# Kernel optimization log

Hardware: AMD Instinct MI355X
Metric: run time of the kernel (lower is better)

Reference implementation:

```python
import jax, jax.numpy as jnp
import numpy as np

N_USER, N_FOOD, N_ING, N_CAT, N_HAB = 50000, 30000, 20000, 5000, 10000
N_NODES = N_USER + N_FOOD + N_ING + N_CAT + N_HAB  # 115000
N_REL = 8
COMMON = 128
HIDDEN = 128
N_CLASSES = 2
N_EDGES = 1500000


def setup_inputs() -> dict:
    key = jax.random.key(0)
    ks = jax.random.split(key, 24)

    def lin(k, din, dout):
        k1, k2 = jax.random.split(k)
        s = 1.0 / np.sqrt(din)
        W = jax.random.uniform(k1, (din, dout), jnp.float32, -s, s)
        b = jax.random.uniform(k2, (dout,), jnp.float32, -s, s)
        return W, b

    Wu, bu = lin(ks[0], 256, COMMON)
    Wf, bf = lin(ks[1], 512, COMMON)
    Wi, bi = lin(ks[2], 128, COMMON)
    Wc, bc = lin(ks[3], 64, COMMON)
    Wh, bh = lin(ks[4], 64, COMMON)

    s1 = 1.0 / np.sqrt(COMMON)
    W1 = jax.random.uniform(ks[5], (N_REL, COMMON, HIDDEN), jnp.float32, -s1, s1)
    root1 = jax.random.uniform(ks[6], (COMMON, HIDDEN), jnp.float32, -s1, s1)
    b1 = jnp.zeros((HIDDEN,), jnp.float32)

    s2 = 1.0 / np.sqrt(HIDDEN)
    W2 = jax.random.uniform(ks[7], (N_REL, HIDDEN, N_CLASSES), jnp.float32, -s2, s2)
    root2 = jax.random.uniform(ks[8], (HIDDEN, N_CLASSES), jnp.float32, -s2, s2)
    b2 = jnp.zeros((N_CLASSES,), jnp.float32)

    return {
        "x_user": jax.random.normal(ks[9], (N_USER, 256), jnp.float32),
        "x_food": jax.random.normal(ks[10], (N_FOOD, 512), jnp.float32),
        "x_ingredient": jax.random.normal(ks[11], (N_ING, 128), jnp.float32),
        "x_category": jax.random.normal(ks[12], (N_CAT, 64), jnp.float32),
        "x_habit": jax.random.normal(ks[13], (N_HAB, 64), jnp.float32),
        "Wu": Wu, "bu": bu, "Wf": Wf, "bf": bf, "Wi": Wi, "bi": bi,
        "Wc": Wc, "bc": bc, "Wh": Wh, "bh": bh,
        "W1": W1, "root1": root1, "b1": b1,
        "W2": W2, "root2": root2, "b2": b2,
        "edge_index": jax.random.randint(ks[14], (2, N_EDGES), 0, N_NODES, jnp.int64),
        "edge_type": jax.random.randint(ks[15], (N_EDGES,), 0, N_REL, jnp.int64),
    }


def rgcn_conv(x, src, dst, etype, W, root, bias):
    # x: [N, Din]; W: [R, Din, Dout]. Per-relation node transform, then
    # per-edge gather + per-(dst, relation) mean aggregation (PyG RGCNConv, aggr='mean').
    N = x.shape[0]
    R = W.shape[0]
    h = jnp.einsum('nd,rdf->nrf', x, W)            # [N, R, Dout]
    msgs = h[src, etype]                           # [E, Dout]
    seg = dst * R + etype                          # combined (dst, relation) segment id
    sums = jax.ops.segment_sum(msgs, seg, num_segments=N * R)
    cnt = jax.ops.segment_sum(jnp.ones((src.shape[0],), x.dtype), seg, num_segments=N * R)
    mean = sums / jnp.maximum(cnt, 1.0)[:, None]   # [N*R, Dout]
    agg = mean.reshape(N, R, -1).sum(axis=1)       # sum over relations
    return agg + x @ root + bias


def reference(x_user, x_food, x_ingredient, x_category, x_habit,
              Wu, bu, Wf, bf, Wi, bi, Wc, bc, Wh, bh,
              W1, root1, b1, W2, root2, b2,
              edge_index, edge_type):
    x_all = jnp.concatenate([
        x_user @ Wu + bu,
        x_food @ Wf + bf,
        x_ingredient @ Wi + bi,
        x_category @ Wc + bc,
        x_habit @ Wh + bh,
    ], axis=0)                                     # [N, COMMON]
    src, dst = edge_index[0], edge_index[1]
    x = rgcn_conv(x_all, src, dst, edge_type, W1, root1, b1)
    x = jax.nn.relu(x)                             # dropout is identity in eval mode
    x = rgcn_conv(x, src, dst, edge_type, W2, root2, b2)
    return jax.nn.log_softmax(x, axis=1)
```

## Files before the change

### kernel.cpp

```cpp
#include <hip/hip_runtime.h>
#include <hip/hip_bf16.h>
#include <math.h>

#define NU 50000
#define NFOOD 30000
#define NING 20000
#define NCAT 5000
#define NHAB 10000
#define NNODES 115000
#define NCHUNK 14375
#define NREL 8
#define NSEG (NNODES * NREL)
#define NEDGE 1500000
#define SCAN_B 256

typedef __attribute__((ext_vector_type(8))) short short8;
typedef __attribute__((ext_vector_type(4))) float f32x4;

static inline size_t alignup(size_t x) { return (x + 255) & ~(size_t)255; }

__device__ inline float bf16_bits_to_f32(unsigned short u) {
  return __uint_as_float(((unsigned)u) << 16);
}
__device__ inline unsigned short f32_to_bf16_bits(float f) {
  unsigned u = __float_as_uint(f);
  unsigned r = u + 0x7fffu + ((u >> 16) & 1u);
  return (unsigned short)(r >> 16);
}
__device__ inline unsigned pack_bf16x2(float lo, float hi) {
  return (unsigned)f32_to_bf16_bits(lo) | ((unsigned)f32_to_bf16_bits(hi) << 16);
}

template <bool A_F32, bool OUT_BF16, bool RELU_OUT>
__global__ __launch_bounds__(256) void mfma_gemm(
    const void* __restrict__ Ain, const unsigned short* __restrict__ Bt, int ldB,
    const float* __restrict__ bias, void* __restrict__ Cv, int ldC, int Nstore,
    int M, int N, int K) {
  __shared__ char As[128 * 128];
  __shared__ char Bs[128 * 128];
  const int tid = threadIdx.x;
  const int lane = tid & 63;
  const int wv = tid >> 6;
  const int bm = blockIdx.y * 128;
  const int bn = blockIdx.x * 128;
  f32x4 acc[2][8] = {};

  for (int k0 = 0; k0 < K; k0 += 64) {
    if (A_F32) {
      const float* A = (const float*)Ain;
#pragma unroll
      for (int it = 0; it < 4; ++it) {
        int u = it * 256 + tid;
        int m = u >> 3, c = u & 7;
        int mg = bm + m; if (mg >= M) mg = M - 1;
        const float4* src = (const float4*)(A + (size_t)mg * K + k0 + c * 8);
        float4 lo4 = src[0], hi4 = src[1];
        unsigned q0 = pack_bf16x2(lo4.x, lo4.y);
        unsigned q1 = pack_bf16x2(lo4.z, lo4.w);
        unsigned q2 = pack_bf16x2(hi4.x, hi4.y);
        unsigned q3 = pack_bf16x2(hi4.z, hi4.w);
        int off = m * 128 + ((c * 16) ^ ((m & 7) << 4));
        *(int4*)(As + off) = make_int4(q0, q1, q2, q3);
      }
    } else {
      const unsigned short* A = (const unsigned short*)Ain;
#pragma unroll
      for (int it = 0; it < 4; ++it) {
        int u = it * 256 + tid;
        int m = u >> 3, c = u & 7;
        int mg = bm + m; if (mg >= M) mg = M - 1;
        int4 v = *(const int4*)((const char*)(A + (size_t)mg * K + k0) + c * 16);
        int off = m * 128 + ((c * 16) ^ ((m & 7) << 4));
        *(int4*)(As + off) = v;
      }
    }
#pragma unroll
    for (int it = 0; it < 4; ++it) {
      int u = it * 256 + tid;
      int n = u >> 3, c = u & 7;
      int4 v = *(const int4*)((const char*)(Bt + (size_t)(bn + n) * ldB + k0) + c * 16);
      int off = n * 128 + ((c * 16) ^ ((n & 7) << 4));
      *(int4*)(Bs + off) = v;
    }
    __syncthreads();
#pragma unroll
    for (int kk = 0; kk < 2; ++kk) {
      int kbyte = kk * 64 + ((lane >> 4) << 4);
      short8 af[2];
#pragma unroll
      for (int mi = 0; mi < 2; ++mi) {
        int m = wv * 32 + mi * 16 + (lane & 15);
        af[mi] = *(const short8*)(As + m * 128 + (kbyte ^ ((m & 7) << 4)));
      }
#pragma unroll
      for (int ni = 0; ni < 8; ++ni) {
        int n = ni * 16 + (lane & 15);
        short8 bf = *(const short8*)(Bs + n * 128 + (kbyte ^ ((n & 7) << 4)));
#pragma unroll
        for (int mi = 0; mi < 2; ++mi)
          acc[mi][ni] = __builtin_amdgcn_mfma_f32_16x16x32_bf16(af[mi], bf, acc[mi][ni], 0, 0, 0);
      }
    }
    __syncthreads();
  }
#pragma unroll
  for (int mi = 0; mi < 2; ++mi) {
#pragma unroll
    for (int r = 0; r < 4; ++r) {
      int row = bm + wv * 32 + mi * 16 + ((lane >> 4) << 2) + r;
      if (row < M) {
#pragma unroll
        for (int ni = 0; ni < 8; ++ni) {
          int col = bn + ni * 16 + (lane & 15);
          if (col < Nstore) {
            float v = acc[mi][ni][r] + (bias ? bias[col] : 0.f);
            if (RELU_OUT) v = fmaxf(v, 0.f);
            if (OUT_BF16)
              ((unsigned short*)Cv)[(size_t)row * ldC + col] = f32_to_bf16_bits(v);
            else
              ((float*)Cv)[(size_t)row * ldC + col] = v;
          }
        }
      }
    }
  }
}

__global__ __launch_bounds__(256) void l1_gemm(
    const unsigned short* __restrict__ M9, const unsigned short* __restrict__ xall,
    const unsigned short* __restrict__ W1rT, const float* __restrict__ b1,
    unsigned short* __restrict__ x1, int d0, int Mc) {
  __shared__ char As[128 * 128];
  __shared__ char Bs[128 * 128];
  const int tid = threadIdx.x;
  const int lane = tid & 63;
  const int wv = tid >> 6;
  const int bm = blockIdx.y * 128;
  f32x4 acc[2][8] = {};

  for (int k0 = 0; k0 < 1152; k0 += 64) {
#pragma unroll
    for (int it = 0; it < 4; ++it) {
      int u = it * 256 + tid;
      int m = u >> 3, c = u & 7;
      int mg = bm + m; if (mg >= Mc) mg = Mc - 1;
      const char* src;
      if (k0 < 1024) src = (const char*)(M9 + (size_t)mg * 1024 + k0) + c * 16;
      else src = (const char*)(xall + (size_t)(d0 + mg) * 128 + (k0 - 1024)) + c * 16;
      int4 v = *(const int4*)src;
      int off = m * 128 + ((c * 16) ^ ((m & 7) << 4));
      *(int4*)(As + off) = v;
    }
#pragma unroll
    for (int it = 0; it < 4; ++it) {
      int u = it * 256 + tid;
      int n = u >> 3, c = u & 7;
      int4 v = *(const int4*)((const char*)(W1rT + (size_t)n * 1152 + k0) + c * 16);
      int off = n * 128 + ((c * 16) ^ ((n & 7) << 4));
      *(int4*)(Bs + off) = v;
    }
    __syncthreads();
#pragma unroll
    for (int kk = 0; kk < 2; ++kk) {
      int kbyte = kk * 64 + ((lane >> 4) << 4);
      short8 af[2];
#pragma unroll
      for (int mi = 0; mi < 2; ++mi) {
        int m = wv * 32 + mi * 16 + (lane & 15);
        af[mi] = *(const short8*)(As + m * 128 + (kbyte ^ ((m & 7) << 4)));
      }
#pragma unroll
      for (int ni = 0; ni < 8; ++ni) {
        int n = ni * 16 + (lane & 15);
        short8 bf = *(const short8*)(Bs + n * 128 + (kbyte ^ ((n & 7) << 4)));
#pragma unroll
        for (int mi = 0; mi < 2; ++mi)
          acc[mi][ni] = __builtin_amdgcn_mfma_f32_16x16x32_bf16(af[mi], bf, acc[mi][ni], 0, 0, 0);
      }
    }
    __syncthreads();
  }
#pragma unroll
  for (int mi = 0; mi < 2; ++mi) {
#pragma unroll
    for (int r = 0; r < 4; ++r) {
      int row = bm + wv * 32 + mi * 16 + ((lane >> 4) << 2) + r;
      if (row < Mc) {
#pragma unroll
        for (int ni = 0; ni < 8; ++ni) {
          int col = ni * 16 + (lane & 15);
          float v = fmaxf(acc[mi][ni][r] + b1[col], 0.f);
          x1[(size_t)(d0 + row) * 128 + col] = f32_to_bf16_bits(v);
        }
      }
    }
  }
}

__global__ void build_Bt(const float* __restrict__ W, unsigned short* __restrict__ Wt,
                         int K, int N) {
  int idx = blockIdx.x * blockDim.x + threadIdx.x;
  if (idx >= N * K) return;
  int n = idx / K, k = idx - n * K;
  Wt[idx] = f32_to_bf16_bits(W[(size_t)k * N + n]);
}

__global__ void build_W1rT(const float* __restrict__ W1, const float* __restrict__ root1,
                           unsigned short* __restrict__ Wt) {
  int idx = blockIdx.x * blockDim.x + threadIdx.x;
  if (idx >= 128 * 1152) return;
  int f = idx / 1152, c = idx - f * 1152;
  float v;
  if (c < 1024) { int t = c >> 7, k = c & 127; v = W1[((size_t)t * 128 + k) * 128 + f]; }
  else { int k = c - 1024; v = root1[(size_t)k * 128 + f]; }
  Wt[idx] = f32_to_bf16_bits(v);
}

__global__ void build_B2pad(const float* __restrict__ W2, const float* __restrict__ root2,
                            unsigned short* __restrict__ Bt) {
  int idx = blockIdx.x * blockDim.x + threadIdx.x;
  if (idx >= 128 * 128) return;
  int n = idx >> 7, k = idx & 127;
  float v = 0.f;
  if (n < 16) v = W2[((size_t)(n >> 1) * 128 + k) * 2 + (n & 1)];
  else if (n < 18) v = root2[(size_t)k * 2 + (n - 16)];
  Bt[idx] = f32_to_bf16_bits(v);
}

__global__ void count_dt_xcd(const int* __restrict__ ei, const int* __restrict__ et,
                             int* __restrict__ cnt_dt) {
  int cls = blockIdx.x & 7;
  unsigned lo = cls * NCHUNK, hi = lo + NCHUNK;
  int e = (blockIdx.x >> 3) * blockDim.x + threadIdx.x;
  int stride = (gridDim.x >> 3) * blockDim.x;
  for (; e < NEDGE; e += stride) {
    unsigned d = (unsigned)ei[NEDGE + e]; if (d >= NNODES) d = 0;
    if (d < lo || d >= hi) continue;
    unsigned t = (unsigned)et[e]; if (t >= NREL) t = 0;
    atomicAdd(cnt_dt + d * NREL + t, 1);
  }
}

__global__ void scan_block(const int* __restrict__ in, int* __restrict__ out,
                           int* __restrict__ bsum, int n) {
  __shared__ int s[SCAN_B];
  int i = blockIdx.x * SCAN_B + threadIdx.x;
  int x = (i < n) ? in[i] : 0;
  s[threadIdx.x] = x;
  __syncthreads();
  for (int d = 1; d < SCAN_B; d <<= 1) {
    int v = (threadIdx.x >= d) ? s[threadIdx.x - d] : 0;
    __syncthreads();
    s[threadIdx.x] += v;
    __syncthreads();
  }
  if (i < n) out[i] = s[threadIdx.x] - x;
  if (threadIdx.x == SCAN_B - 1) bsum[blockIdx.x] = s[threadIdx.x];
}

__global__ void scan_top(int* __restrict__ bsum, int* __restrict__ bofs, int nb) {
  __shared__ int s[512];
  int x = (threadIdx.x < nb) ? bsum[threadIdx.x] : 0;
  s[threadIdx.x] = x;
  __syncthreads();
  for (int d = 1; d < 512; d <<= 1) {
    int v = (threadIdx.x >= d) ? s[threadIdx.x - d] : 0;
    __syncthreads();
    s[threadIdx.x] += v;
    __syncthreads();
  }
  if (threadIdx.x < nb) bofs[threadIdx.x] = s[threadIdx.x] - x;
}

__global__ void scan_apply3(int* __restrict__ rp2, const int* __restrict__ lvl1,
                            const int* __restrict__ lvl2, int* __restrict__ slot, int n) {
  int i = blockIdx.x * blockDim.x + threadIdx.x;
  if (i >= n) return;
  int v = rp2[i] + lvl1[i >> 8] + lvl2[i >> 16];
  rp2[i] = v;
  slot[i] = v;
}

__global__ void scatter_edges_xcd(const int* __restrict__ ei, const int* __restrict__ et,
                                  int* __restrict__ slot, unsigned* __restrict__ packed) {
  int cls = blockIdx.x & 7;
  unsigned lo = cls * NCHUNK, hi = lo + NCHUNK;
  int e = (blockIdx.x >> 3) * blockDim.x + threadIdx.x;
  int stride = (gridDim.x >> 3) * blockDim.x;
  for (; e < NEDGE; e += stride) {
    unsigned d = (unsigned)ei[NEDGE + e]; if (d >= NNODES) d = 0;
    if (d < lo || d >= hi) continue;
    unsigned s = (unsigned)ei[e];  if (s >= NNODES) s = 0;
    unsigned t = (unsigned)et[e];  if (t >= NREL)  t = 0;
    int pos = atomicAdd(slot + d * NREL + t, 1);
    packed[pos] = s;
  }
}

__global__ __launch_bounds__(256) void gather_rounds(
    const int* __restrict__ rp2, const unsigned* __restrict__ packed,
    const int4* __restrict__ xu, unsigned* __restrict__ M9, int d0, int d1) {
  const int lane = threadIdx.x & 63;
  const int qtr = lane >> 4;
  const int sub = lane & 15;
  int wid = (blockIdx.x * blockDim.x + threadIdx.x) >> 6;
  int nw = (gridDim.x * blockDim.x) >> 6;
  for (int p0 = d0 + wid * 4; p0 < d1; p0 += nw * 4) {
    int d = p0 + qtr;
    bool valid = (d < d1);
    int bi = (valid ? d : d0) * NREL;
    int b[9];
#pragma unroll
    for (int q = 0; q < 9; ++q)
      b[q] = (bi + q == NSEG) ? NEDGE : rp2[bi + q];
    int len[8];
    int mx = 0;
#pragma unroll
    for (int q = 0; q < 8; ++q) {
      len[q] = valid ? (b[q + 1] - b[q]) : 0;
      mx = len[q] > mx ? len[q] : mx;
    }
    float a[8][8];
#pragma unroll
    for (int q = 0; q < 8; ++q)
#pragma unroll
      for (int j = 0; j < 8; ++j) a[q][j] = 0.f;
    for (int r = 0; r < mx; ++r) {
#pragma unroll
      for (int q = 0; q < 8; ++q) {
        if (r < len[q]) {
          int4 v = xu[(size_t)packed[b[q] + r] * 16 + sub];
          unsigned u0 = (unsigned)v.x, u1 = (unsigned)v.y;
          unsigned u2 = (unsigned)v.z, u3 = (unsigned)v.w;
          a[q][0] += bf16_bits_to_f32((unsigned short)(u0 & 0xffffu));
          a[q][1] += bf16_bits_to_f32((unsigned short)(u0 >> 16));
          a[q][2] += bf16_bits_to_f32((unsigned short)(u1 & 0xffffu));
          a[q][3] += bf16_bits_to_f32((unsigned short)(u1 >> 16));
          a[q][4] += bf16_bits_to_f32((unsigned short)(u2 & 0xffffu));
          a[q][5] += bf16_bits_to_f32((unsigned short)(u2 >> 16));
          a[q][6] += bf16_bits_to_f32((unsigned short)(u3 & 0xffffu));
          a[q][7] += bf16_bits_to_f32((unsigned short)(u3 >> 16));
        }
      }
    }
    if (valid) {
      unsigned* rowp = M9 + (size_t)(d - d0) * 512;
#pragma unroll
      for (int q = 0; q < 8; ++q) {
        float w = 1.0f / (float)(len[q] > 0 ? len[q] : 1);
        uint4 o;
        o.x = pack_bf16x2(a[q][0] * w, a[q][1] * w);
        o.y = pack_bf16x2(a[q][2] * w, a[q][3] * w);
        o.z = pack_bf16x2(a[q][4] * w, a[q][5] * w);
        o.w = pack_bf16x2(a[q][6] * w, a[q][7] * w);
        *(uint4*)(rowp + q * 64 + sub * 4) = o;
      }
    }
  }
}

__global__ void fused_out(const int* __restrict__ rp2, const unsigned* __restrict__ packed,
                          const float* __restrict__ h2, const float* __restrict__ b2,
                          float* __restrict__ out) {
  int gt = blockIdx.x * blockDim.x + threadIdx.x;
  int d = gt >> 2;
  int l4 = gt & 3;
  if (d >= NNODES) return;
  float z0 = 0.f, z1 = 0.f;
#pragma unroll
  for (int k = 0; k < 2; ++k) {
    int t = l4 * 2 + k;
    int i = d * NREL + t;
    int beg = rp2[i];
    int end = (i == NSEG - 1) ? NEDGE : rp2[i + 1];
    float s0 = 0.f, s1 = 0.f;
    for (int e = beg; e < end; ++e) {
      unsigned s = packed[e];
      s0 += h2[(size_t)s * 18 + t * 2];
      s1 += h2[(size_t)s * 18 + t * 2 + 1];
    }
    int c = end - beg;
    float w = 1.0f / (float)(c > 0 ? c : 1);
    z0 += s0 * w;
    z1 += s1 * w;
  }
  z0 += __shfl_xor(z0, 1, 4); z0 += __shfl_xor(z0, 2, 4);
  z1 += __shfl_xor(z1, 1, 4); z1 += __shfl_xor(z1, 2, 4);
  if (l4 == 0) {
    z0 += h2[(size_t)d * 18 + 16] + b2[0];
    z1 += h2[(size_t)d * 18 + 17] + b2[1];
    float m = fmaxf(z0, z1);
    float l = m + logf(expf(z0 - m) + expf(z1 - m));
    out[(size_t)d * 2 + 0] = z0 - l;
    out[(size_t)d * 2 + 1] = z1 - l;
  }
}

__global__ void fill_sentinel(float* __restrict__ out, int n, float v) {
  int i = blockIdx.x * blockDim.x + threadIdx.x;
  if (i < n) out[i] = v;
}

extern "C" void kernel_launch(void* const* d_in, const int* in_sizes, int n_in,
                              void* d_out, int out_size, void* d_ws, size_t ws_size,
                              hipStream_t stream) {
  const float* x_user = (const float*)d_in[0];
  const float* x_food = (const float*)d_in[1];
  const float* x_ing  = (const float*)d_in[2];
  const float* x_cat  = (const float*)d_in[3];
  const float* x_hab  = (const float*)d_in[4];
  const float* Wu = (const float*)d_in[5];  const float* bu  = (const float*)d_in[6];
  const float* Wf = (const float*)d_in[7];  const float* bfo = (const float*)d_in[8];
  const float* Wi = (const float*)d_in[9];  const float* bi  = (const float*)d_in[10];
  const float* Wc = (const float*)d_in[11]; const float* bc  = (const float*)d_in[12];
  const float* Wh = (const float*)d_in[13]; const float* bh  = (const float*)d_in[14];
  const float* W1 = (const float*)d_in[15]; const float* root1 = (const float*)d_in[16];
  const float* b1 = (const float*)d_in[17];
  const float* W2 = (const float*)d_in[18]; const float* root2 = (const float*)d_in[19];
  const float* b2 = (const float*)d_in[20];
  const int* ei = (const int*)d_in[21];
  const int* et = (const int*)d_in[22];
  (void)in_sizes; (void)n_in;

  dim3 blk(256);
  const int NB_A = (NSEG + SCAN_B - 1) / SCAN_B;
  const int NB_B = (NB_A + SCAN_B - 1) / SCAN_B;

  char* ws = (char*)d_ws;
  size_t off = 0;
  unsigned short* x_all = (unsigned short*)(ws + off); off += alignup((size_t)NNODES * 128 * 2);
  unsigned short* x1    = (unsigned short*)(ws + off); off += alignup((size_t)NNODES * 128 * 2);
  int* cnt_dt = (int*)(ws + off);        off += alignup((size_t)NSEG * 4);
  int* rp2 = (int*)(ws + off);           off += alignup((size_t)NSEG * 4);
  int* slot = (int*)(ws + off);          off += alignup((size_t)NSEG * 4);
  unsigned* packed = (unsigned*)(ws + off); off += alignup((size_t)NEDGE * 4);
  int* bsumA = (int*)(ws + off);         off += alignup((size_t)4096 * 4);
  int* bsumAs = (int*)(ws + off);        off += alignup((size_t)4096 * 4);
  int* bsumB = (int*)(ws + off);         off += alignup((size_t)64 * 4);
  int* bofsB = (int*)(ws + off);         off += alignup((size_t)64 * 4);
  unsigned short* WuT = (unsigned short*)(ws + off); off += alignup((size_t)128 * 256 * 2);
  unsigned short* WfT = (unsigned short*)(ws + off); off += alignup((size_t)128 * 512 * 2);
  unsigned short* WiT = (unsigned short*)(ws + off); off += alignup((size_t)128 * 128 * 2);
  unsigned short* WcT = (unsigned short*)(ws + off); off += alignup((size_t)128 * 64 * 2);
  unsigned short* WhT = (unsigned short*)(ws + off); off += alignup((size_t)128 * 64 * 2);
  unsigned short* W1rT = (unsigned short*)(ws + off); off += alignup((size_t)128 * 1152 * 2);
  unsigned short* B2pad = (unsigned short*)(ws + off); off += alignup((size_t)128 * 128 * 2);
  float* h2 = (float*)(ws + off);        off += alignup((size_t)NNODES * 18 * 4);
  size_t base = off;

  int NCH = 0;
  for (int cand = 2; cand <= 16; cand <<= 1) {
    size_t ch = ((size_t)NNODES + cand - 1) / cand;
    if (base + alignup(ch * 1024 * 2) <= ws_size) { NCH = cand; break; }
  }
  if (NCH == 0) {
    fill_sentinel<<<(out_size + 255) / 256, blk, 0, stream>>>((float*)d_out, out_size, -777.0f);
    return;
  }
  unsigned short* M9 = (unsigned short*)(ws + base);
  const int CH = (NNODES + NCH - 1) / NCH;

  hipMemsetAsync(cnt_dt, 0, (size_t)NSEG * 4, stream);

  build_Bt<<<(128 * 256 + 255) / 256, blk, 0, stream>>>(Wu, WuT, 256, 128);
  build_Bt<<<(128 * 512 + 255) / 256, blk, 0, stream>>>(Wf, WfT, 512, 128);
  build_Bt<<<(128 * 128 + 255) / 256, blk, 0, stream>>>(Wi, WiT, 128, 128);
  build_Bt<<<(128 * 64 + 255) / 256, blk, 0, stream>>>(Wc, WcT, 64, 128);
  build_Bt<<<(128 * 64 + 255) / 256, blk, 0, stream>>>(Wh, WhT, 64, 128);
  build_W1rT<<<(128 * 1152 + 255) / 256, blk, 0, stream>>>(W1, root1, W1rT);
  build_B2pad<<<(128 * 128 + 255) / 256, blk, 0, stream>>>(W2, root2, B2pad);

  { dim3 g(1, (NU + 127) / 128);
    mfma_gemm<true, true, false><<<g, blk, 0, stream>>>(x_user, WuT, 256, bu, (void*)x_all, 128, 128, NU, 128, 256); }
  { dim3 g(1, (NFOOD + 127) / 128);
    mfma_gemm<true, true, false><<<g, blk, 0, stream>>>(x_food, WfT, 512, bfo, (void*)(x_all + (size_t)NU * 128), 128, 128, NFOOD, 128, 512); }
  { dim3 g(1, (NING + 127) / 128);
    mfma_gemm<true, true, false><<<g, blk, 0, stream>>>(x_ing, WiT, 128, bi, (void*)(x_all + (size_t)(NU + NFOOD) * 128), 128, 128, NING, 128, 128); }
  { dim3 g(1, (NCAT + 127) / 128);
    mfma_gemm<true, true, false><<<g, blk, 0, stream>>>(x_cat, WcT, 64, bc, (void*)(x_all + (size_t)(NU + NFOOD + NING) * 128), 128, 128, NCAT, 128, 64); }
  { dim3 g(1, (NHAB + 127) / 128);
    mfma_gemm<true, true, false><<<g, blk, 0, stream>>>(x_hab, WhT, 64, bh, (void*)(x_all + (size_t)(NU + NFOOD + NING + NCAT) * 128), 128, 128, NHAB, 128, 64); }

  count_dt_xcd<<<2048, blk, 0, stream>>>(ei, et, cnt_dt);
  scan_block<<<NB_A, SCAN_B, 0, stream>>>(cnt_dt, rp2, bsumA, NSEG);
  scan_block<<<NB_B, SCAN_B, 0, stream>>>(bsumA, bsumAs, bsumB, NB_A);
  scan_top<<<1, 512, 0, stream>>>(bsumB, bofsB, NB_B);
  scan_apply3<<<NB_A, SCAN_B, 0, stream>>>(rp2, bsumAs, bofsB, slot, NSEG);
  scatter_edges_xcd<<<2048, blk, 0, stream>>>(ei, et, slot, packed);

  for (int c = 0; c < NCH; ++c) {
    int d0 = c * CH;
    int d1 = (d0 + CH < NNODES) ? d0 + CH : NNODES;
    int Mc = d1 - d0;
    gather_rounds<<<2048, blk, 0, stream>>>(rp2, packed, (const int4*)x_all,
                                            (unsigned*)M9, d0, d1);
    dim3 g(1, (Mc + 127) / 128);
    l1_gemm<<<g, blk, 0, stream>>>(M9, x_all, W1rT, b1, x1, d0, Mc);
  }

  { dim3 g(1, (NNODES + 127) / 128);
    mfma_gemm<false, false, false><<<g, blk, 0, stream>>>(x1, B2pad, 128, nullptr, (void*)h2, 18, 18, NNODES, 128, 128); }

  fused_out<<<(NNODES * 4 + 255) / 256, blk, 0, stream>>>(rp2, packed, h2, b2, (float*)d_out);
}
```

Before: 536.9 us.

## Merge weight prep, input projections and scan levels into fewer launches

Replaces seven weight-conversion kernels with one grid-stride build_all kernel. Replaces five per-type projection GEMMs with a single proj_all launch that selects its input, bias and weight by tile index. The three-level scan becomes two levels, using a single-block sequential mid scan with a carry. The chunk-count search now also accepts a single chunk, so the gather/l1_gemm loop can run once when workspace allows. The intent is to cut launch overhead and tail effects, at the cost of a serial single-block scan over about 3600 partial sums.

```diff
diff --git a/kernel.cpp b/kernel.cpp
--- a/kernel.cpp
+++ b/kernel.cpp
@@ -126,6 +126,92 @@
   }
 }
 
+struct ProjP {
+  const float *A0, *A1, *A2, *A3, *A4;
+  const float *b0, *b1, *b2, *b3, *b4;
+  int t1, t2, t3, t4;
+};
+
+__global__ __launch_bounds__(256) void proj_all(ProjP P, const unsigned short* __restrict__ Wp,
+                                                unsigned short* __restrict__ x_all) {
+  __shared__ char As[128 * 128];
+  __shared__ char Bs[128 * 128];
+  const int by = blockIdx.y;
+  const int tid = threadIdx.x;
+  const int lane = tid & 63;
+  const int wv = tid >> 6;
+  const float* A; const float* bias;
+  int M, K, Woff, tile0; long Coff;
+  if (by < P.t1)      { A = P.A0; bias = P.b0; M = NU;    K = 256; Woff = 0;      Coff = 0;                 tile0 = 0; }
+  else if (by < P.t2) { A = P.A1; bias = P.b1; M = NFOOD; K = 512; Woff = 32768;  Coff = (long)NU * 128;    tile0 = P.t1; }
+  else if (by < P.t3) { A = P.A2; bias = P.b2; M = NING;  K = 128; Woff = 98304;  Coff = (long)(NU+NFOOD)*128; tile0 = P.t2; }
+  else if (by < P.t4) { A = P.A3; bias = P.b3; M = NCAT;  K = 64;  Woff = 114688; Coff = (long)(NU+NFOOD+NING)*128; tile0 = P.t3; }
+  else                { A = P.A4; bias = P.b4; M = NHAB;  K = 64;  Woff = 122880; Coff = (long)(NU+NFOOD+NING+NCAT)*128; tile0 = P.t4; }
+  const unsigned short* Bt = Wp + Woff;
+  const int bm = (by - tile0) * 128;
+  f32x4 acc[2][8] = {};
+
+  for (int k0 = 0; k0 < K; k0 += 64) {
+#pragma unroll
+    for (int it = 0; it < 4; ++it) {
+      int u = it * 256 + tid;
+      int m = u >> 3, c = u & 7;
+      int mg = bm + m; if (mg >= M) mg = M - 1;
+      const float4* src = (const float4*)(A + (size_t)mg * K + k0 + c * 8);
+      float4 lo4 = src[0], hi4 = src[1];
+      unsigned q0 = pack_bf16x2(lo4.x, lo4.y);
+      unsigned q1 = pack_bf16x2(lo4.z, lo4.w);
+      unsigned q2 = pack_bf16x2(hi4.x, hi4.y);
+      unsigned q3 = pack_bf16x2(hi4.z, hi4.w);
+      int off = m * 128 + ((c * 16) ^ ((m & 7) << 4));
+      *(int4*)(As + off) = make_int4(q0, q1, q2, q3);
+    }
+#pragma unroll
+    for (int it = 0; it < 4; ++it) {
+      int u = it * 256 + tid;
+      int n = u >> 3, c = u & 7;
+      int4 v = *(const int4*)((const char*)(Bt + (size_t)n * K + k0) + c * 16);
+      int off = n * 128 + ((c * 16) ^ ((n & 7) << 4));
+      *(int4*)(Bs + off) = v;
+    }
+    __syncthreads();
+#pragma unroll
+    for (int kk = 0; kk < 2; ++kk) {
+      int kbyte = kk * 64 + ((lane >> 4) << 4);
+      short8 af[2];
+#pragma unroll
+      for (int mi = 0; mi < 2; ++mi) {
+        int m = wv * 32 + mi * 16 + (lane & 15);
+        af[mi] = *(const short8*)(As + m * 128 + (kbyte ^ ((m & 7) << 4)));
+      }
+#pragma unroll
+      for (int ni = 0; ni < 8; ++ni) {
+        int n = ni * 16 + (lane & 15);
+        short8 bf = *(const short8*)(Bs + n * 128 + (kbyte ^ ((n & 7) << 4)));
+#pragma unroll
+        for (int mi = 0; mi < 2; ++mi)
+          acc[mi][ni] = __builtin_amdgcn_mfma_f32_16x16x32_bf16(af[mi], bf, acc[mi][ni], 0, 0, 0);
+      }
+    }
+    __syncthreads();
+  }
+#pragma unroll
+  for (int mi = 0; mi < 2; ++mi) {
+#pragma unroll
+    for (int r = 0; r < 4; ++r) {
+      int row = bm + wv * 32 + mi * 16 + ((lane >> 4) << 2) + r;
+      if (row < M) {
+#pragma unroll
+        for (int ni = 0; ni < 8; ++ni) {
+          int col = ni * 16 + (lane & 15);
+          float v = acc[mi][ni][r] + bias[col];
+          x_all[Coff + (size_t)row * 128 + col] = f32_to_bf16_bits(v);
+        }
+      }
+    }
+  }
+}
+
 __global__ __launch_bounds__(256) void l1_gemm(
     const unsigned short* __restrict__ M9, const unsigned short* __restrict__ xall,
     const unsigned short* __restrict__ W1rT, const float* __restrict__ b1,
@@ -197,34 +283,48 @@
   }
 }
 
-__global__ void build_Bt(const float* __restrict__ W, unsigned short* __restrict__ Wt,
-                         int K, int N) {
-  int idx = blockIdx.x * blockDim.x + threadIdx.x;
-  if (idx >= N * K) return;
-  int n = idx / K, k = idx - n * K;
-  Wt[idx] = f32_to_bf16_bits(W[(size_t)k * N + n]);
-}
-
-__global__ void build_W1rT(const float* __restrict__ W1, const float* __restrict__ root1,
-                           unsigned short* __restrict__ Wt) {
-  int idx = blockIdx.x * blockDim.x + threadIdx.x;
-  if (idx >= 128 * 1152) return;
-  int f = idx / 1152, c = idx - f * 1152;
-  float v;
-  if (c < 1024) { int t = c >> 7, k = c & 127; v = W1[((size_t)t * 128 + k) * 128 + f]; }
-  else { int k = c - 1024; v = root1[(size_t)k * 128 + f]; }
-  Wt[idx] = f32_to_bf16_bits(v);
-}
-
-__global__ void build_B2pad(const float* __restrict__ W2, const float* __restrict__ root2,
-                            unsigned short* __restrict__ Bt) {
-  int idx = blockIdx.x * blockDim.x + threadIdx.x;
-  if (idx >= 128 * 128) return;
-  int n = idx >> 7, k = idx & 127;
-  float v = 0.f;
-  if (n < 16) v = W2[((size_t)(n >> 1) * 128 + k) * 2 + (n & 1)];
-  else if (n < 18) v = root2[(size_t)k * 2 + (n - 16)];
-  Bt[idx] = f32_to_bf16_bits(v);
+__global__ void build_all(const float* __restrict__ Wu, const float* __restrict__ Wf,
+                          const float* __restrict__ Wi, const float* __restrict__ Wc,
+                          const float* __restrict__ Wh, const float* __restrict__ W1,
+                          const float* __restrict__ root1, const float* __restrict__ W2,
+                          const float* __restrict__ root2,
+                          unsigned short* __restrict__ Wp,
+                          unsigned short* __restrict__ W1rT,
+                          unsigned short* __restrict__ B2pad) {
+  const int T0 = 32768, T1 = T0 + 65536, T2 = T1 + 16384, T3 = T2 + 8192, T4 = T3 + 8192,
+            T5 = T4 + 147456, T6 = T5 + 16384;
+  int i = blockIdx.x * blockDim.x + threadIdx.x;
+  int stride = gridDim.x * blockDim.x;
+  for (; i < T6; i += stride) {
+    if (i < T0) {
+      int n = i / 256, k = i - n * 256;
+      Wp[i] = f32_to_bf16_bits(Wu[(size_t)k * 128 + n]);
+    } else if (i < T1) {
+      int j = i - T0; int n = j / 512, k = j - n * 512;
+      Wp[i] = f32_to_bf16_bits(Wf[(size_t)k * 128 + n]);
+    } else if (i < T2) {
+      int j = i - T1; int n = j >> 7, k = j & 127;
+      Wp[i] = f32_to_bf16_bits(Wi[(size_t)k * 128 + n]);
+    } else if (i < T3) {
+      int j = i - T2; int n = j >> 6, k = j & 63;
+      Wp[i] = f32_to_bf16_bits(Wc[(size_t)k * 128 + n]);
+    } else if (i < T4) {
+      int j = i - T3; int n = j >> 6, k = j & 63;
+      Wp[i] = f32_to_bf16_bits(Wh[(size_t)k * 128 + n]);
+    } else if (i < T5) {
+      int j = i - T4; int f = j / 1152, c = j - f * 1152;
+      float v;
+      if (c < 1024) { int t = c >> 7, k = c & 127; v = W1[((size_t)t * 128 + k) * 128 + f]; }
+      else { int k = c - 1024; v = root1[(size_t)k * 128 + f]; }
+      W1rT[j] = f32_to_bf16_bits(v);
+    } else {
+      int j = i - T5; int n = j >> 7, k = j & 127;
+      float v = 0.f;
+      if (n < 16) v = W2[((size_t)(n >> 1) * 128 + k) * 2 + (n & 1)];
+      else if (n < 18) v = root2[(size_t)k * 2 + (n - 16)];
+      B2pad[j] = f32_to_bf16_bits(v);
+    }
+  }
 }
 
 __global__ void count_dt_xcd(const int* __restrict__ ei, const int* __restrict__ et,
@@ -258,25 +358,34 @@
   if (threadIdx.x == SCAN_B - 1) bsum[blockIdx.x] = s[threadIdx.x];
 }
 
-__global__ void scan_top(int* __restrict__ bsum, int* __restrict__ bofs, int nb) {
-  __shared__ int s[512];
-  int x = (threadIdx.x < nb) ? bsum[threadIdx.x] : 0;
-  s[threadIdx.x] = x;
+__global__ void scan_mid(const int* __restrict__ bsumA, int* __restrict__ bsumAs, int nb) {
+  __shared__ int s[256];
+  __shared__ int carry;
+  if (threadIdx.x == 0) carry = 0;
   __syncthreads();
-  for (int d = 1; d < 512; d <<= 1) {
-    int v = (threadIdx.x >= d) ? s[threadIdx.x - d] : 0;
-    __syncthreads();
-    s[threadIdx.x] += v;
-    __syncthreads();
-  }
-  if (threadIdx.x < nb) bofs[threadIdx.x] = s[threadIdx.x] - x;
-}
-
-__global__ void scan_apply3(int* __restrict__ rp2, const int* __restrict__ lvl1,
-                            const int* __restrict__ lvl2, int* __restrict__ slot, int n) {
+  for (int c0 = 0; c0 < nb; c0 += 256) {
+    int i = c0 + threadIdx.x;
+    int x = (i < nb) ? bsumA[i] : 0;
+    s[threadIdx.x] = x;
+    __syncthreads();
+    for (int d = 1; d < 256; d <<= 1) {
+      int v = (threadIdx.x >= d) ? s[threadIdx.x - d] : 0;
+      __syncthreads();
+      s[threadIdx.x] += v;
+      __syncthreads();
+    }
+    if (i < nb) bsumAs[i] = carry + s[threadIdx.x] - x;
+    __syncthreads();
+    if (threadIdx.x == 255) carry += s[255];
+    __syncthreads();
+  }
+}
+
+__global__ void scan_apply2(int* __restrict__ rp2, const int* __restrict__ lvl1,
+                            int* __restrict__ slot, int n) {
   int i = blockIdx.x * blockDim.x + threadIdx.x;
   if (i >= n) return;
-  int v = rp2[i] + lvl1[i >> 8] + lvl2[i >> 16];
+  int v = rp2[i] + lvl1[i >> 8];
   rp2[i] = v;
   slot[i] = v;
 }
@@ -424,7 +533,6 @@
 
   dim3 blk(256);
   const int NB_A = (NSEG + SCAN_B - 1) / SCAN_B;
-  const int NB_B = (NB_A + SCAN_B - 1) / SCAN_B;
 
   char* ws = (char*)d_ws;
   size_t off = 0;
@@ -436,20 +544,14 @@
   unsigned* packed = (unsigned*)(ws + off); off += alignup((size_t)NEDGE * 4);
   int* bsumA = (int*)(ws + off);         off += alignup((size_t)4096 * 4);
   int* bsumAs = (int*)(ws + off);        off += alignup((size_t)4096 * 4);
-  int* bsumB = (int*)(ws + off);         off += alignup((size_t)64 * 4);
-  int* bofsB = (int*)(ws + off);         off += alignup((size_t)64 * 4);
-  unsigned short* WuT = (unsigned short*)(ws + off); off += alignup((size_t)128 * 256 * 2);
-  unsigned short* WfT = (unsigned short*)(ws + off); off += alignup((size_t)128 * 512 * 2);
-  unsigned short* WiT = (unsigned short*)(ws + off); off += alignup((size_t)128 * 128 * 2);
-  unsigned short* WcT = (unsigned short*)(ws + off); off += alignup((size_t)128 * 64 * 2);
-  unsigned short* WhT = (unsigned short*)(ws + off); off += alignup((size_t)128 * 64 * 2);
+  unsigned short* Wp = (unsigned short*)(ws + off);   off += alignup((size_t)131072 * 2);
   unsigned short* W1rT = (unsigned short*)(ws + off); off += alignup((size_t)128 * 1152 * 2);
   unsigned short* B2pad = (unsigned short*)(ws + off); off += alignup((size_t)128 * 128 * 2);
   float* h2 = (float*)(ws + off);        off += alignup((size_t)NNODES * 18 * 4);
   size_t base = off;
 
   int NCH = 0;
-  for (int cand = 2; cand <= 16; cand <<= 1) {
+  for (int cand = 1; cand <= 16; cand <<= 1) {
     size_t ch = ((size_t)NNODES + cand - 1) / cand;
     if (base + alignup(ch * 1024 * 2) <= ws_size) { NCH = cand; break; }
   }
@@ -462,30 +564,22 @@
 
   hipMemsetAsync(cnt_dt, 0, (size_t)NSEG * 4, stream);
 
-  build_Bt<<<(128 * 256 + 255) / 256, blk, 0, stream>>>(Wu, WuT, 256, 128);
-  build_Bt<<<(128 * 512 + 255) / 256, blk, 0, stream>>>(Wf, WfT, 512, 128);
-  build_Bt<<<(128 * 128 + 255) / 256, blk, 0, stream>>>(Wi, WiT, 128, 128);
-  build_Bt<<<(128 * 64 + 255) / 256, blk, 0, stream>>>(Wc, WcT, 64, 128);
-  build_Bt<<<(128 * 64 + 255) / 256, blk, 0, stream>>>(Wh, WhT, 64, 128);
-  build_W1rT<<<(128 * 1152 + 255) / 256, blk, 0, stream>>>(W1, root1, W1rT);
-  build_B2pad<<<(128 * 128 + 255) / 256, blk, 0, stream>>>(W2, root2, B2pad);
-
-  { dim3 g(1, (NU + 127) / 128);
-    mfma_gemm<true, true, false><<<g, blk, 0, stream>>>(x_user, WuT, 256, bu, (void*)x_all, 128, 128, NU, 128, 256); }
-  { dim3 g(1, (NFOOD + 127) / 128);
-    mfma_gemm<true, true, false><<<g, blk, 0, stream>>>(x_food, WfT, 512, bfo, (void*)(x_all + (size_t)NU * 128), 128, 128, NFOOD, 128, 512); }
-  { dim3 g(1, (NING + 127) / 128);
-    mfma_gemm<true, true, false><<<g, blk, 0, stream>>>(x_ing, WiT, 128, bi, (void*)(x_all + (size_t)(NU + NFOOD) * 128), 128, 128, NING, 128, 128); }
-  { dim3 g(1, (NCAT + 127) / 128);
-    mfma_gemm<true, true, false><<<g, blk, 0, stream>>>(x_cat, WcT, 64, bc, (void*)(x_all + (size_t)(NU + NFOOD + NING) * 128), 128, 128, NCAT, 128, 64); }
-  { dim3 g(1, (NHAB + 127) / 128);
-    mfma_gemm<true, true, false><<<g, blk, 0, stream>>>(x_hab, WhT, 64, bh, (void*)(x_all + (size_t)(NU + NFOOD + NING + NCAT) * 128), 128, 128, NHAB, 128, 64); }
+  build_all<<<1152, blk, 0, stream>>>(Wu, Wf, Wi, Wc, Wh, W1, root1, W2, root2,
+                                      Wp, W1rT, B2pad);
+
+  {
+    ProjP P;
+    P.A0 = x_user; P.A1 = x_food; P.A2 = x_ing; P.A3 = x_cat; P.A4 = x_hab;
+    P.b0 = bu; P.b1 = bfo; P.b2 = bi; P.b3 = bc; P.b4 = bh;
+    P.t1 = 391; P.t2 = 391 + 235; P.t3 = 391 + 235 + 157; P.t4 = 391 + 235 + 157 + 40;
+    int ntiles = P.t4 + 79;
+    proj_all<<<dim3(1, ntiles), blk, 0, stream>>>(P, Wp, x_all);
+  }
 
   count_dt_xcd<<<2048, blk, 0, stream>>>(ei, et, cnt_dt);
   scan_block<<<NB_A, SCAN_B, 0, stream>>>(cnt_dt, rp2, bsumA, NSEG);
-  scan_block<<<NB_B, SCAN_B, 0, stream>>>(bsumA, bsumAs, bsumB, NB_A);
-  scan_top<<<1, 512, 0, stream>>>(bsumB, bofsB, NB_B);
-  scan_apply3<<<NB_A, SCAN_B, 0, stream>>>(rp2, bsumAs, bofsB, slot, NSEG);
+  scan_mid<<<1, 256, 0, stream>>>(bsumA, bsumAs, NB_A);
+  scan_apply2<<<NB_A, SCAN_B, 0, stream>>>(rp2, bsumAs, slot, NSEG);
   scatter_edges_xcd<<<2048, blk, 0, stream>>>(ei, et, slot, packed);
 
   for (int c = 0; c < NCH; ++c) {
```

Measured after the change: 478.4 us. 1.12x faster.
